# Performance work log

Measured on AMD Instinct MI355X. Metric: run time of the kernel, lower is better.

The kernel has to match this reference:

```python
import jax, jax.numpy as jnp
import numpy as np

B, T, S, H, V, L = 32, 64, 128, 512, 32000, 2  # batch, tgt_len, src_len, d_model, vocab, n_layers


def setup_inputs() -> dict:
    key = jax.random.key(0)
    ks = jax.random.split(key, 14)
    sc = 1.0 / np.sqrt(H)
    tgt = jax.random.randint(ks[0], (B, T), 0, V, dtype=jnp.int32)
    h0 = jax.random.normal(ks[1], (L, B, H), jnp.float32)
    c0 = jax.random.normal(ks[2], (L, B, H), jnp.float32)
    encoder_outputs = jax.random.normal(ks[3], (B, S, H), jnp.float32)
    emb = (jax.random.normal(ks[4], (V, H), jnp.float32) * 0.02).at[0].set(0.0)  # pad_idx=0 row zeroed
    W_ih = jax.random.normal(ks[5], (L, 4 * H, H), jnp.float32) * sc  # gate order i,f,g,o (torch)
    W_hh = jax.random.normal(ks[6], (L, 4 * H, H), jnp.float32) * sc
    b_ih = jax.random.normal(ks[7], (L, 4 * H), jnp.float32) * sc
    b_hh = jax.random.normal(ks[8], (L, 4 * H), jnp.float32) * sc
    Wc = jax.random.normal(ks[9], (H, 2 * H), jnp.float32) * sc
    bc = jax.random.normal(ks[10], (H,), jnp.float32) * sc
    Wo = jax.random.normal(ks[11], (V, H), jnp.float32) * sc
    bo = jax.random.normal(ks[12], (V,), jnp.float32) * sc
    return dict(tgt=tgt, h0=h0, c0=c0, encoder_outputs=encoder_outputs, emb=emb,
                W_ih=W_ih, W_hh=W_hh, b_ih=b_ih, b_hh=b_hh, Wc=Wc, bc=bc, Wo=Wo, bo=bo)


def reference(tgt, h0, c0, encoder_outputs, emb, W_ih, W_hh, b_ih, b_hh, Wc, bc, Wo, bo):
    n_layers = W_ih.shape[0]

    def step(carry, token):
        h, c = carry  # each [L, B, H]
        x = emb[token]  # [B, H]
        hs, cs = [], []
        for l in range(n_layers):  # small fixed structural loop
            gates = x @ W_ih[l].T + b_ih[l] + h[l] @ W_hh[l].T + b_hh[l]  # [B, 4H]
            i_g, f_g, g_g, o_g = jnp.split(gates, 4, axis=-1)
            c_new = jax.nn.sigmoid(f_g) * c[l] + jax.nn.sigmoid(i_g) * jnp.tanh(g_g)
            h_new = jax.nn.sigmoid(o_g) * jnp.tanh(c_new)
            hs.append(h_new)
            cs.append(c_new)
            x = h_new
        out = x  # [B, H] top-layer output
        # Luong (dot) attention over encoder outputs
        scores = jnp.einsum('bh,bsh->bs', out, encoder_outputs)
        attn = jax.nn.softmax(scores, axis=-1)
        context = jnp.einsum('bs,bsh->bh', attn, encoder_outputs)
        out_att = jnp.tanh(jnp.concatenate([out, context], axis=-1) @ Wc.T + bc)
        pred = out_att @ Wo.T + bo  # [B, V]
        return (jnp.stack(hs), jnp.stack(cs)), pred

    (h, c), preds = jax.lax.scan(step, (h0, c0), tgt.T)  # scan over time (T-major)
    return preds.transpose(1, 0, 2), h, c  # [B, T, V], hidden state
```

## Files before the change

### kernel.cpp

```cpp
#include <hip/hip_runtime.h>
#include <hip/hip_bf16.h>

#define Bz 32
#define Tz 64
#define Sz 128
#define Hz 512
#define Vz 32000
#define G4 2048
#define NBLK 256
#define NPH 65

#define A_RLX __ATOMIC_RELAXED
#define SC_AG __HIP_MEMORY_SCOPE_AGENT

using bf16x8 = __attribute__((ext_vector_type(8))) short;
using f32x4  = __attribute__((ext_vector_type(4))) float;

__device__ __forceinline__ unsigned short f2bf(float f){
  unsigned int u = __float_as_uint(f);
  u += 0x7fffu + ((u >> 16) & 1u);
  return (unsigned short)(u >> 16);
}
__device__ __forceinline__ float sigf(float x){ return 1.f/(1.f + expf(-x)); }

__device__ __forceinline__ void stc(float* p, float v){
  __hip_atomic_store(p, v, A_RLX, SC_AG);
}
__device__ __forceinline__ float ldc(const float* p){
  return __hip_atomic_load(p, A_RLX, SC_AG);
}

__device__ __forceinline__ void gbar(unsigned* bar, int bid, unsigned* ep){
  asm volatile("s_waitcnt vmcnt(0)" ::: "memory");
  __syncthreads();
  const unsigned e = ++(*ep);
  const int tid = threadIdx.x;
  const int g = bid >> 4, m = bid & 15;
  if (m != 0){
    if (tid == 0){
      __hip_atomic_store(&bar[g*16 + m], e, A_RLX, SC_AG);
      while (__hip_atomic_load(&bar[576 + bid*16], A_RLX, SC_AG) != e)
        __builtin_amdgcn_s_sleep(1);
    }
  } else {
    if (tid >= 1 && tid <= 15){
      while (__hip_atomic_load(&bar[g*16 + tid], A_RLX, SC_AG) != e)
        __builtin_amdgcn_s_sleep(1);
    }
    __syncthreads();
    if (bid == 0){
      if (tid == 0) __hip_atomic_store(&bar[256 + 0], e, A_RLX, SC_AG);
      if (tid < 16){
        while (__hip_atomic_load(&bar[256 + tid], A_RLX, SC_AG) != e)
          __builtin_amdgcn_s_sleep(1);
      }
      __syncthreads();
      if (tid < 16) __hip_atomic_store(&bar[320 + tid*16], e, A_RLX, SC_AG);
    } else {
      if (tid == 0){
        __hip_atomic_store(&bar[256 + g], e, A_RLX, SC_AG);
        while (__hip_atomic_load(&bar[320 + g*16], A_RLX, SC_AG) != e)
          __builtin_amdgcn_s_sleep(1);
      }
      __syncthreads();
    }
    if (tid < 16) __hip_atomic_store(&bar[576 + (g*16 + tid)*16], e, A_RLX, SC_AG);
    if (tid == 0){
      while (__hip_atomic_load(&bar[576 + bid*16], A_RLX, SC_AG) != e)
        __builtin_amdgcn_s_sleep(1);
    }
  }
  __syncthreads();
  __builtin_amdgcn_sched_barrier(0);
}

__device__ __forceinline__ void xreduce(float (&a)[32], int lane){
  #pragma unroll
  for (int j = 0; j < 32; j++) a[j] += __shfl_xor(a[j], 32);
  #pragma unroll
  for (int st = 0; st < 5; st++){
    const int o = 16 >> st;
    bool hi = (lane & o) != 0;
    float tmp[16];
    #pragma unroll
    for (int j = 0; j < o; j++){
      float lo_v = a[j], hi_v = a[j + o];
      float sent = hi ? lo_v : hi_v;
      float recv = __shfl_xor(sent, o);
      tmp[j] = (hi ? hi_v : lo_v) + recv;
    }
    #pragma unroll
    for (int j = 0; j < o; j++) a[j] = tmp[j];
  }
}

__device__ __forceinline__ void stage2c(float* dA, const float* sA,
                                        float* dB, const float* sB, int tid){
  #pragma unroll
  for (int h = 0; h < 2; h++){
    float ra[16], rb[16];
    #pragma unroll
    for (int i = 0; i < 16; i++) ra[i] = ldc(sA + tid + (h*16 + i)*512);
    #pragma unroll
    for (int i = 0; i < 16; i++) rb[i] = ldc(sB + tid + (h*16 + i)*512);
    #pragma unroll
    for (int i = 0; i < 16; i++){
      int f = tid + (h*16 + i)*512;
      dA[(f >> 9)*520 + (f & 511)] = ra[i];
    }
    #pragma unroll
    for (int i = 0; i < 16; i++){
      int f = tid + (h*16 + i)*512;
      dB[(f >> 9)*520 + (f & 511)] = rb[i];
    }
  }
}

__global__ __launch_bounds__(256) void init_state_v7(const float* __restrict__ h0,
    float* __restrict__ h0p, float* __restrict__ h1p, unsigned int* __restrict__ bar){
  int i = blockIdx.x*256 + threadIdx.x;
  if (i < 16384) h0p[16384 + i] = h0[i];
  else           h1p[3*16384 + (i - 16384)] = h0[i];
  if (i < 4704) bar[i] = 0u;
}

__global__ __launch_bounds__(256) void conv_bf16_kernel(const float* __restrict__ src,
    unsigned short* __restrict__ dst){
  int i = (blockIdx.x*256 + threadIdx.x)*4;
  float4 v = *(const float4*)(src + i);
  ushort4 o;
  o.x = f2bf(v.x); o.y = f2bf(v.y); o.z = f2bf(v.z); o.w = f2bf(v.w);
  *(ushort4*)(dst + i) = o;
}

__global__ __launch_bounds__(256) void pack_l0_v3(const float* __restrict__ W,
    float* __restrict__ out){
  int idx4 = blockIdx.x*256 + threadIdx.x;
  int r = idx4 >> 7, k4 = idx4 & 127;
  int srow = (r & 3)*Hz + (r >> 2);
  ((float4*)out)[idx4] = ((const float4*)W)[srow*128 + k4];
}
__global__ __launch_bounds__(256) void pack_l1_v3(const float* __restrict__ Wi,
    const float* __restrict__ Wh, float* __restrict__ out){
  int idx4 = blockIdx.x*256 + threadIdx.x;
  int r = idx4 >> 8, k4 = idx4 & 255;
  int srow = (r & 3)*Hz + (r >> 2);
  float4 v = (k4 < 128) ? ((const float4*)Wi)[srow*128 + k4]
                        : ((const float4*)Wh)[srow*128 + (k4 - 128)];
  ((float4*)out)[idx4] = v;
}

__global__ __launch_bounds__(256) void x0g_v3(const int* __restrict__ tgt,
    const float* __restrict__ emb, const float* __restrict__ W,
    const float* __restrict__ bi, const float* __restrict__ bh,
    float* __restrict__ out){
  __shared__ float As[32][68], Bs[32][68];
  __shared__ int tok_s[64];
  int tid = threadIdx.x;
  int m0 = blockIdx.y*64, n0 = blockIdx.x*64;
  if (tid < 64){ int tb = m0 + tid; tok_s[tid] = tgt[(tb & 31)*Tz + (tb >> 5)]; }
  __syncthreads();
  int lm = tid >> 2, lk = (tid & 3)*8;
  int ty = tid >> 4, tx = tid & 15;
  float acc[4][4] = {{0.f}};
  for (int kt = 0; kt < 16; kt++){
    float4 a0 = *(const float4*)(emb + (size_t)tok_s[lm]*Hz + kt*32 + lk);
    float4 a1 = *(const float4*)(emb + (size_t)tok_s[lm]*Hz + kt*32 + lk + 4);
    float4 b0 = *(const float4*)(W   + (size_t)(n0+lm)*Hz + kt*32 + lk);
    float4 b1 = *(const float4*)(W   + (size_t)(n0+lm)*Hz + kt*32 + lk + 4);
    __syncthreads();
    As[lk+0][lm]=a0.x; As[lk+1][lm]=a0.y; As[lk+2][lm]=a0.z; As[lk+3][lm]=a0.w;
    As[lk+4][lm]=a1.x; As[lk+5][lm]=a1.y; As[lk+6][lm]=a1.z; As[lk+7][lm]=a1.w;
    Bs[lk+0][lm]=b0.x; Bs[lk+1][lm]=b0.y; Bs[lk+2][lm]=b0.z; Bs[lk+3][lm]=b0.w;
    Bs[lk+4][lm]=b1.x; Bs[lk+5][lm]=b1.y; Bs[lk+6][lm]=b1.z; Bs[lk+7][lm]=b1.w;
    __syncthreads();
    #pragma unroll
    for (int k = 0; k < 32; k++){
      float4 av = *(const float4*)&As[k][ty*4];
      float4 bv = *(const float4*)&Bs[k][tx*4];
      acc[0][0]+=av.x*bv.x; acc[0][1]+=av.x*bv.y; acc[0][2]+=av.x*bv.z; acc[0][3]+=av.x*bv.w;
      acc[1][0]+=av.y*bv.x; acc[1][1]+=av.y*bv.y; acc[1][2]+=av.y*bv.z; acc[1][3]+=av.y*bv.w;
      acc[2][0]+=av.z*bv.x; acc[2][1]+=av.z*bv.y; acc[2][2]+=av.z*bv.z; acc[2][3]+=av.z*bv.w;
      acc[3][0]+=av.w*bv.x; acc[3][1]+=av.w*bv.y; acc[3][2]+=av.w*bv.z; acc[3][3]+=av.w*bv.w;
    }
  }
  #pragma unroll
  for (int j = 0; j < 4; j++){
    int col = n0 + tx*4 + j;
    float bias = bi[col] + bh[col];
    #pragma unroll
    for (int i = 0; i < 4; i++){
      int tb = m0 + ty*4 + i;
      int tt = tb >> 5, bb = tb & 31;
      out[((size_t)tt*2048 + col)*32 + bb] = acc[i][j] + bias;
    }
  }
}

__global__ __launch_bounds__(512, 1) void decoder_persist_v7(
    const float* __restrict__ Wp0, const float* __restrict__ Wp1,
    const float* x0gT,
    const float* __restrict__ bi1, const float* __restrict__ bh1,
    const float* __restrict__ c0in,
    float* __restrict__ h0p,
    float* __restrict__ h1p,
    float* hist,
    float* __restrict__ cbuf,
    unsigned* __restrict__ bar){
  extern __shared__ float sm[];
  float* hstA = sm;
  float* hstB = sm + 16640;
  float* gsA  = sm + 33280;
  float* gsB  = sm + 33792;
  float4* hA4 = (float4*)hstA;
  float4* hB4 = (float4*)hstB;

  const int bid = blockIdx.x, tid = threadIdx.x;
  const int w4 = tid >> 6, lane = tid & 63;
  const int kh = w4 >> 2, rpair = w4 & 3;
  const int r0 = bid*8 + rpair*2, r1 = r0 + 1;
  unsigned ep = 0;

  const float4* Wp0_4 = (const float4*)Wp0;
  const float4* Wp1_4 = (const float4*)Wp1;
  float4 w0A  = Wp0_4[r0*128 + kh*64 + lane];
  float4 w0B  = Wp0_4[r1*128 + kh*64 + lane];
  float4 w1xA = Wp1_4[r0*256 +       kh*64 + lane];
  float4 w1xB = Wp1_4[r1*256 +       kh*64 + lane];
  float4 w1hA = Wp1_4[r0*256 + 128 + kh*64 + lane];
  float4 w1hB = Wp1_4[r1*256 + 128 + kh*64 + lane];
  float bs_i=0.f, bs_f=0.f, bs_g=0.f, bs_o=0.f;
  float c0_reg=0.f, c1_reg=0.f;
  if (tid < 64){
    int b = tid & 31, u = bid*2 + (tid >> 5);
    bs_i = bi1[u]        + bh1[u];
    bs_f = bi1[512+u]    + bh1[512+u];
    bs_g = bi1[1024+u]   + bh1[1024+u];
    bs_o = bi1[1536+u]   + bh1[1536+u];
    c0_reg = c0in[b*512 + u];
    c1_reg = c0in[16384 + b*512 + u];
  }
  __syncthreads();

  for (int tau = 0; tau < NPH; ++tau){
    stage2c(hstA, h0p + ((tau+1)&1)*16384, hstB, h1p + ((tau+2)&3)*16384, tid);
    float xgi=0.f, xgf=0.f, xgg=0.f, xgo=0.f;
    if (tau < 64 && tid < 64){
      int b = tid & 31, u = bid*2 + (tid >> 5);
      const float* xg = x0gT + (size_t)tau*65536;
      xgi = xg[(u       )*32 + b];
      xgf = xg[(512  + u)*32 + b];
      xgg = xg[(1024 + u)*32 + b];
      xgo = xg[(1536 + u)*32 + b];
    }
    __syncthreads();
    {
      float aL0A[32], aL0B[32], aL1A[32], aL1B[32];
      #pragma unroll
      for (int b = 0; b < 32; b++){ aL0A[b]=0.f; aL0B[b]=0.f; aL1A[b]=0.f; aL1B[b]=0.f; }
      const float4* pA = hA4 + kh*64 + lane;
      const float4* pB = hB4 + kh*64 + lane;
      #pragma unroll
      for (int b = 0; b < 32; b++){
        float4 ha = pA[b*130];
        float4 hb = pB[b*130];
        aL0A[b] = fmaf(ha.x,w0A.x, fmaf(ha.y,w0A.y, fmaf(ha.z,w0A.z, fmaf(ha.w,w0A.w, aL0A[b]))));
        aL0B[b] = fmaf(ha.x,w0B.x, fmaf(ha.y,w0B.y, fmaf(ha.z,w0B.z, fmaf(ha.w,w0B.w, aL0B[b]))));
        float t1 = fmaf(ha.x,w1xA.x, fmaf(ha.y,w1xA.y, fmaf(ha.z,w1xA.z, fmaf(ha.w,w1xA.w, aL1A[b]))));
        aL1A[b] = fmaf(hb.x,w1hA.x, fmaf(hb.y,w1hA.y, fmaf(hb.z,w1hA.z, fmaf(hb.w,w1hA.w, t1))));
        float t2 = fmaf(ha.x,w1xB.x, fmaf(ha.y,w1xB.y, fmaf(ha.z,w1xB.z, fmaf(ha.w,w1xB.w, aL1B[b]))));
        aL1B[b] = fmaf(hb.x,w1hB.x, fmaf(hb.y,w1hB.y, fmaf(hb.z,w1hB.z, fmaf(hb.w,w1hB.w, t2))));
      }
      xreduce(aL0A, lane); xreduce(aL0B, lane);
      gsA[kh*256 + (rpair*2 + (lane >= 32 ? 1 : 0))*32 + (lane & 31)] = (lane < 32) ? aL0A[0] : aL0B[0];
      xreduce(aL1A, lane); xreduce(aL1B, lane);
      gsB[kh*256 + (rpair*2 + (lane >= 32 ? 1 : 0))*32 + (lane & 31)] = (lane < 32) ? aL1A[0] : aL1B[0];
    }
    __syncthreads();
    if (tid < 64){
      int ul = tid >> 5, b = tid & 31, u = bid*2 + ul, rl = ul*4;
      if (tau < 64){
        float gi = gsA[(rl+0)*32+b] + gsA[256+(rl+0)*32+b] + xgi;
        float gf = gsA[(rl+1)*32+b] + gsA[256+(rl+1)*32+b] + xgf;
        float gg = gsA[(rl+2)*32+b] + gsA[256+(rl+2)*32+b] + xgg;
        float go = gsA[(rl+3)*32+b] + gsA[256+(rl+3)*32+b] + xgo;
        float cn = sigf(gf)*c0_reg + sigf(gi)*tanhf(gg);
        c0_reg = cn;
        stc(h0p + (tau&1)*16384 + b*512 + u, sigf(go)*tanhf(cn));
      }
      if (tau >= 1){
        int t1s = tau - 1;
        float gi = gsB[(rl+0)*32+b] + gsB[256+(rl+0)*32+b] + bs_i;
        float gf = gsB[(rl+1)*32+b] + gsB[256+(rl+1)*32+b] + bs_f;
        float gg = gsB[(rl+2)*32+b] + gsB[256+(rl+2)*32+b] + bs_g;
        float go = gsB[(rl+3)*32+b] + gsB[256+(rl+3)*32+b] + bs_o;
        float cn = sigf(gf)*c1_reg + sigf(gi)*tanhf(gg);
        c1_reg = cn;
        float hv = sigf(go)*tanhf(cn);
        stc(h1p + (t1s&3)*16384 + b*512 + u, hv);
        hist[(size_t)t1s*65536 + b*512 + u] = hv;
      }
    }
    gbar(bar, bid, &ep);
  }
  if (tid < 64){
    int b = tid & 31, u = bid*2 + (tid >> 5);
    cbuf[b*512 + u] = c0_reg;
    cbuf[16384 + b*512 + u] = c1_reg;
  }
}

__global__ __launch_bounds__(256) void attn_batch(const float* hist,
    const float* __restrict__ enc, float* ctxout){
  __shared__ float h_s[Hz], e_s[Sz], red_s[2];
  const int bid = blockIdx.x;
  const int t = bid >> 5, b = bid & 31, tid = threadIdx.x;
  const float* h1 = hist + (size_t)t*65536 + b*512;
  *(float2*)(h_s + tid*2) = *(const float2*)(h1 + tid*2);
  __syncthreads();
  {
    int s = tid >> 1, half = tid & 1;
    const float4* e4 = (const float4*)(enc + ((size_t)b*Sz + s)*Hz + half*256);
    const float4* h4 = (const float4*)(h_s + half*256);
    float a = 0.f;
    #pragma unroll 16
    for (int k = 0; k < 64; k++){
      float4 e = e4[k], h = h4[k];
      a += e.x*h.x + e.y*h.y + e.z*h.z + e.w*h.w;
    }
    a += __shfl_xor(a, 1);
    if (!half) e_s[s] = a;
  }
  __syncthreads();
  if (tid < 64){
    float v = fmaxf(e_s[tid], e_s[tid+64]);
    #pragma unroll
    for (int o = 32; o; o >>= 1) v = fmaxf(v, __shfl_xor(v, o));
    if (tid == 0) red_s[0] = v;
  }
  __syncthreads();
  if (tid < Sz) e_s[tid] = expf(e_s[tid] - red_s[0]);
  __syncthreads();
  if (tid < 64){
    float v = e_s[tid] + e_s[tid+64];
    #pragma unroll
    for (int o = 32; o; o >>= 1) v += __shfl_xor(v, o);
    if (tid == 0) red_s[1] = v;
  }
  __syncthreads();
  {
    float inv = 1.f/red_s[1];
    int k0 = tid*2;
    float c0 = 0.f, c1 = 0.f;
    const float* ep = enc + (size_t)b*Sz*Hz + k0;
    #pragma unroll 8
    for (int s = 0; s < Sz; s++){
      float2 ev = *(const float2*)(ep + (size_t)s*Hz);
      float pr = e_s[s];
      c0 += pr*ev.x; c1 += pr*ev.y;
    }
    float2 o; o.x = c0*inv; o.y = c1*inv;
    *(float2*)(ctxout + (size_t)t*65536 + 32768 + b*512 + k0) = o;
  }
}

__global__ __launch_bounds__(256) void outatt_gemm(const float* xg,
    const float* __restrict__ Wc, const float* __restrict__ bc,
    unsigned short* __restrict__ oa){
  __shared__ float As[32][68], Bs[32][68];
  int tid = threadIdx.x;
  int m0 = blockIdx.y*64, n0 = blockIdx.x*64;
  int lm = tid >> 2, lk = (tid & 3)*8;
  int ty = tid >> 4, tx = tid & 15;
  int am = m0 + lm, at = am >> 5, ab = am & 31;
  const float* arow = xg + (size_t)at*65536 + ab*512;
  float acc[4][4] = {{0.f}};
  for (int kt = 0; kt < 32; kt++){
    int k = kt*32 + lk;
    const float* asrc = (k < 512) ? (arow + k) : (arow + 32768 + (k - 512));
    float4 a0 = *(const float4*)asrc;
    float4 a1 = *(const float4*)(asrc + 4);
    float4 b0 = *(const float4*)(Wc + (size_t)(n0+lm)*1024 + k);
    float4 b1 = *(const float4*)(Wc + (size_t)(n0+lm)*1024 + k + 4);
    __syncthreads();
    As[lk+0][lm]=a0.x; As[lk+1][lm]=a0.y; As[lk+2][lm]=a0.z; As[lk+3][lm]=a0.w;
    As[lk+4][lm]=a1.x; As[lk+5][lm]=a1.y; As[lk+6][lm]=a1.z; As[lk+7][lm]=a1.w;
    Bs[lk+0][lm]=b0.x; Bs[lk+1][lm]=b0.y; Bs[lk+2][lm]=b0.z; Bs[lk+3][lm]=b0.w;
    Bs[lk+4][lm]=b1.x; Bs[lk+5][lm]=b1.y; Bs[lk+6][lm]=b1.z; Bs[lk+7][lm]=b1.w;
    __syncthreads();
    #pragma unroll
    for (int k2 = 0; k2 < 32; k2++){
      float4 av = *(const float4*)&As[k2][ty*4];
      float4 bv = *(const float4*)&Bs[k2][tx*4];
      acc[0][0]+=av.x*bv.x; acc[0][1]+=av.x*bv.y; acc[0][2]+=av.x*bv.z; acc[0][3]+=av.x*bv.w;
      acc[1][0]+=av.y*bv.x; acc[1][1]+=av.y*bv.y; acc[1][2]+=av.y*bv.z; acc[1][3]+=av.y*bv.w;
      acc[2][0]+=av.z*bv.x; acc[2][1]+=av.z*bv.y; acc[2][2]+=av.z*bv.z; acc[2][3]+=av.z*bv.w;
      acc[3][0]+=av.w*bv.x; acc[3][1]+=av.w*bv.y; acc[3][2]+=av.w*bv.z; acc[3][3]+=av.w*bv.w;
    }
  }
  #pragma unroll
  for (int j = 0; j < 4; j++){
    int col = n0 + tx*4 + j;
    float bias = bc[col];
    #pragma unroll
    for (int i = 0; i < 4; i++){
      int m = m0 + ty*4 + i;
      int t = m >> 5, b = m & 31;
      oa[((size_t)(b*64 + t))*512 + col] = f2bf(tanhf(acc[i][j] + bias));
    }
  }
}

__global__ __launch_bounds__(256) void pred_gemm_v2(const unsigned short* __restrict__ A,
    const unsigned short* __restrict__ Bm, const float* __restrict__ bo,
    float* __restrict__ out){
  __shared__ unsigned short As[128*32];
  __shared__ unsigned short Bs[128*32];
  int bid = blockIdx.x;
  int xcd = bid & 7, lin = bid >> 3;
  int ntile = xcd*32 + (lin & 31);
  int mtile = lin >> 5;
  if (ntile >= 250) return;
  int n0 = ntile*128, m0 = mtile*128;
  int tid = threadIdx.x, lane = tid & 63, wid = tid >> 6;
  f32x4 acc[4][4];
  #pragma unroll
  for (int i = 0; i < 4; i++)
    #pragma unroll
    for (int j = 0; j < 4; j++)
      #pragma unroll
      for (int r = 0; r < 4; r++) acc[i][j][r] = 0.f;

  int wm = wid >> 1, wn = wid & 1;
  int r16 = lane & 15, kgr = lane >> 4;

  for (int kt = 0; kt < Hz/32; kt++){
    __syncthreads();
    #pragma unroll
    for (int call = 0; call < 2; call++){
      int c = call*256 + tid;
      int row = c >> 2, kg = c & 3;
      int kgs = kg ^ ((row >> 1) & 3);
      *(int4*)&As[row*32 + kgs*8] = *(const int4*)(A  + (size_t)(m0+row)*Hz + kt*32 + kg*8);
      *(int4*)&Bs[row*32 + kgs*8] = *(const int4*)(Bm + (size_t)(n0+row)*Hz + kt*32 + kg*8);
    }
    __syncthreads();
    bf16x8 aF[4], bF[4];
    #pragma unroll
    for (int i = 0; i < 4; i++){
      int ra = wm*64 + i*16 + r16;
      int rb = wn*64 + i*16 + r16;
      aF[i] = *(const bf16x8*)&As[ra*32 + (kgr ^ ((ra>>1)&3))*8];
      bF[i] = *(const bf16x8*)&Bs[rb*32 + (kgr ^ ((rb>>1)&3))*8];
    }
    #pragma unroll
    for (int i = 0; i < 4; i++)
      #pragma unroll
      for (int j = 0; j < 4; j++)
        acc[i][j] = __builtin_amdgcn_mfma_f32_16x16x32_bf16(aF[i], bF[j], acc[i][j], 0, 0, 0);
  }

  int rg = lane >> 4;
  #pragma unroll
  for (int i = 0; i < 4; i++)
    #pragma unroll
    for (int j = 0; j < 4; j++){
      int col = n0 + wn*64 + j*16 + r16;
      float bias = bo[col];
      #pragma unroll
      for (int r = 0; r < 4; r++){
        int row = m0 + wm*64 + i*16 + rg*4 + r;
        out[(size_t)row*Vz + col] = acc[i][j][r] + bias;
      }
    }
}

__global__ __launch_bounds__(256) void copy_hc_v4(const float* __restrict__ h0fin,
    const float* __restrict__ h1fin, const float* __restrict__ cbuf,
    float* __restrict__ out_hc){
  int i = blockIdx.x*256 + threadIdx.x;
  float v;
  if (i < 16384)      v = h0fin[i];
  else if (i < 32768) v = h1fin[i-16384];
  else                v = cbuf[i-32768];
  out_hc[i] = v;
}

extern "C" void kernel_launch(void* const* d_in, const int* in_sizes, int n_in,
                              void* d_out, int out_size, void* d_ws, size_t ws_size,
                              hipStream_t stream){
  const int*   tgt = (const int*)  d_in[0];
  const float* h0  = (const float*)d_in[1];
  const float* c0  = (const float*)d_in[2];
  const float* enc = (const float*)d_in[3];
  const float* emb = (const float*)d_in[4];
  const float* Wih = (const float*)d_in[5];
  const float* Whh = (const float*)d_in[6];
  const float* bih = (const float*)d_in[7];
  const float* bhh = (const float*)d_in[8];
  const float* Wc  = (const float*)d_in[9];
  const float* bc  = (const float*)d_in[10];
  const float* Wo  = (const float*)d_in[11];
  const float* bo  = (const float*)d_in[12];
  float* out = (float*)d_out;

  float* x0g  = (float*)d_ws;
  float* h0p  = x0g  + 4194304;
  float* h1p  = h0p  + 32768;
  float* cbuf = h1p  + 65536;
  float* Wp0  = cbuf + 32768;
  float* Wp1  = Wp0  + 1048576;
  unsigned int* bar = (unsigned int*)(Wp1 + 2097152);
  unsigned short* oa    = (unsigned short*)(bar + 4704);
  unsigned short* wo_bf = oa + 1048576;

  const int DLDS_BYTES = 34304 * 4;
  hipFuncSetAttribute((const void*)decoder_persist_v7,
      hipFuncAttributeMaxDynamicSharedMemorySize, DLDS_BYTES);

  init_state_v7<<<128, 256, 0, stream>>>(h0, h0p, h1p, bar);
  conv_bf16_kernel<<<16000, 256, 0, stream>>>(Wo, wo_bf);
  pack_l0_v3<<<1024, 256, 0, stream>>>(Whh, Wp0);
  pack_l1_v3<<<2048, 256, 0, stream>>>(Wih + (size_t)G4*Hz, Whh + (size_t)G4*Hz, Wp1);
  x0g_v3<<<dim3(32, 32), 256, 0, stream>>>(tgt, emb, Wih, bih, bhh, x0g);

  decoder_persist_v7<<<NBLK, 512, DLDS_BYTES, stream>>>(
      Wp0, Wp1, x0g, bih + G4, bhh + G4, c0,
      h0p, h1p, x0g, cbuf, (unsigned int*)bar);

  attn_batch<<<2048, 256, 0, stream>>>(x0g, enc, x0g);
  outatt_gemm<<<dim3(8, 32), 256, 0, stream>>>(x0g, Wc, bc, oa);
  pred_gemm_v2<<<4096, 256, 0, stream>>>(oa, wo_bf, bo, out);
  copy_hc_v4<<<256, 256, 0, stream>>>(h0p + 16384, x0g + (size_t)63*65536, cbuf,
                                      out + (size_t)Bz*Tz*Vz);

  (void)in_sizes; (void)n_in; (void)out_size; (void)ws_size;
}
```

Measured before the change: 1.190 ms.

## Flatten grid barrier to single-level master gather and broadcast

Replaces the two-level hierarchical grid barrier (16 groups of 16 blocks, then a group-leader exchange) with a flat barrier. Block 0 polls 256 per-block arrival flags in parallel, one thread per block, then broadcasts release flags on separate cache lines. This cuts the number of serial round trips per barrier. The trade-off is more concurrent polling on block 0. The state-staging copy is also restructured to issue all 32 loads per array before any stores, which raises register use to get more memory-level parallelism.

```diff
diff --git a/kernel.cpp b/kernel.cpp
--- a/kernel.cpp
+++ b/kernel.cpp
@@ -35,38 +35,18 @@
   __syncthreads();
   const unsigned e = ++(*ep);
   const int tid = threadIdx.x;
-  const int g = bid >> 4, m = bid & 15;
-  if (m != 0){
+  if (bid == 0){
+    if (tid >= 1 && tid < 256){
+      while (__hip_atomic_load(&bar[tid*4], A_RLX, SC_AG) != e)
+        __builtin_amdgcn_s_sleep(1);
+    }
+    __syncthreads();
+    if (tid < 256)
+      __hip_atomic_store(&bar[1024 + tid*16], e, A_RLX, SC_AG);
+  } else {
     if (tid == 0){
-      __hip_atomic_store(&bar[g*16 + m], e, A_RLX, SC_AG);
-      while (__hip_atomic_load(&bar[576 + bid*16], A_RLX, SC_AG) != e)
-        __builtin_amdgcn_s_sleep(1);
-    }
-  } else {
-    if (tid >= 1 && tid <= 15){
-      while (__hip_atomic_load(&bar[g*16 + tid], A_RLX, SC_AG) != e)
-        __builtin_amdgcn_s_sleep(1);
-    }
-    __syncthreads();
-    if (bid == 0){
-      if (tid == 0) __hip_atomic_store(&bar[256 + 0], e, A_RLX, SC_AG);
-      if (tid < 16){
-        while (__hip_atomic_load(&bar[256 + tid], A_RLX, SC_AG) != e)
-          __builtin_amdgcn_s_sleep(1);
-      }
-      __syncthreads();
-      if (tid < 16) __hip_atomic_store(&bar[320 + tid*16], e, A_RLX, SC_AG);
-    } else {
-      if (tid == 0){
-        __hip_atomic_store(&bar[256 + g], e, A_RLX, SC_AG);
-        while (__hip_atomic_load(&bar[320 + g*16], A_RLX, SC_AG) != e)
-          __builtin_amdgcn_s_sleep(1);
-      }
-      __syncthreads();
-    }
-    if (tid < 16) __hip_atomic_store(&bar[576 + (g*16 + tid)*16], e, A_RLX, SC_AG);
-    if (tid == 0){
-      while (__hip_atomic_load(&bar[576 + bid*16], A_RLX, SC_AG) != e)
+      __hip_atomic_store(&bar[bid*4], e, A_RLX, SC_AG);
+      while (__hip_atomic_load(&bar[1024 + bid*16], A_RLX, SC_AG) != e)
         __builtin_amdgcn_s_sleep(1);
     }
   }
@@ -96,32 +76,29 @@
 
 __device__ __forceinline__ void stage2c(float* dA, const float* sA,
                                         float* dB, const float* sB, int tid){
-  #pragma unroll
-  for (int h = 0; h < 2; h++){
-    float ra[16], rb[16];
-    #pragma unroll
-    for (int i = 0; i < 16; i++) ra[i] = ldc(sA + tid + (h*16 + i)*512);
-    #pragma unroll
-    for (int i = 0; i < 16; i++) rb[i] = ldc(sB + tid + (h*16 + i)*512);
-    #pragma unroll
-    for (int i = 0; i < 16; i++){
-      int f = tid + (h*16 + i)*512;
-      dA[(f >> 9)*520 + (f & 511)] = ra[i];
-    }
-    #pragma unroll
-    for (int i = 0; i < 16; i++){
-      int f = tid + (h*16 + i)*512;
-      dB[(f >> 9)*520 + (f & 511)] = rb[i];
-    }
-  }
-}
-
-__global__ __launch_bounds__(256) void init_state_v7(const float* __restrict__ h0,
+  float ra[32], rb[32];
+  #pragma unroll
+  for (int i = 0; i < 32; i++) ra[i] = ldc(sA + tid + i*512);
+  #pragma unroll
+  for (int i = 0; i < 32; i++) rb[i] = ldc(sB + tid + i*512);
+  #pragma unroll
+  for (int i = 0; i < 32; i++){
+    int f = tid + i*512;
+    dA[(f >> 9)*520 + (f & 511)] = ra[i];
+  }
+  #pragma unroll
+  for (int i = 0; i < 32; i++){
+    int f = tid + i*512;
+    dB[(f >> 9)*520 + (f & 511)] = rb[i];
+  }
+}
+
+__global__ __launch_bounds__(256) void init_state_v8(const float* __restrict__ h0,
     float* __restrict__ h0p, float* __restrict__ h1p, unsigned int* __restrict__ bar){
   int i = blockIdx.x*256 + threadIdx.x;
   if (i < 16384) h0p[16384 + i] = h0[i];
   else           h1p[3*16384 + (i - 16384)] = h0[i];
-  if (i < 4704) bar[i] = 0u;
+  if (i < 5120) bar[i] = 0u;
 }
 
 __global__ __launch_bounds__(256) void conv_bf16_kernel(const float* __restrict__ src,
@@ -197,7 +174,7 @@
   }
 }
 
-__global__ __launch_bounds__(512, 1) void decoder_persist_v7(
+__global__ __launch_bounds__(512, 1) void decoder_persist_v8(
     const float* __restrict__ Wp0, const float* __restrict__ Wp1,
     const float* x0gT,
     const float* __restrict__ bi1, const float* __restrict__ bh1,
@@ -511,20 +488,20 @@
   float* Wp0  = cbuf + 32768;
   float* Wp1  = Wp0  + 1048576;
   unsigned int* bar = (unsigned int*)(Wp1 + 2097152);
-  unsigned short* oa    = (unsigned short*)(bar + 4704);
+  unsigned short* oa    = (unsigned short*)(bar + 5120);
   unsigned short* wo_bf = oa + 1048576;
 
   const int DLDS_BYTES = 34304 * 4;
-  hipFuncSetAttribute((const void*)decoder_persist_v7,
+  hipFuncSetAttribute((const void*)decoder_persist_v8,
       hipFuncAttributeMaxDynamicSharedMemorySize, DLDS_BYTES);
 
-  init_state_v7<<<128, 256, 0, stream>>>(h0, h0p, h1p, bar);
+  init_state_v8<<<128, 256, 0, stream>>>(h0, h0p, h1p, bar);
   conv_bf16_kernel<<<16000, 256, 0, stream>>>(Wo, wo_bf);
   pack_l0_v3<<<1024, 256, 0, stream>>>(Whh, Wp0);
   pack_l1_v3<<<2048, 256, 0, stream>>>(Wih + (size_t)G4*Hz, Whh + (size_t)G4*Hz, Wp1);
   x0g_v3<<<dim3(32, 32), 256, 0, stream>>>(tgt, emb, Wih, bih, bhh, x0g);
 
-  decoder_persist_v7<<<NBLK, 512, DLDS_BYTES, stream>>>(
+  decoder_persist_v8<<<NBLK, 512, DLDS_BYTES, stream>>>(
       Wp0, Wp1, x0g, bih + G4, bhh + G4, c0,
       h0p, h1p, x0g, cbuf, (unsigned int*)bar);
 
```

Result: faster. 1.115 ms (median of 2 runs) (-6.3%).
